# Kernel optimization log

Measured on AMD Instinct MI355X. Metric: run time of the kernel, lower is better.

The kernel has to match this reference:

```python
import jax, jax.numpy as jnp
import numpy as np

D_IN = 768      # encoder feature dim (hardcoded in GRUCell(768, d_model))
D_MODEL = 256   # hidden size
B, T = 64, 512


def _gru_cell(x, h, W_ih, W_hh, b_ih, b_hh):
    # PyTorch GRUCell math. W_ih: [in, 3H], W_hh: [H, 3H], biases [3H].
    gi = x @ W_ih + b_ih
    gh = h @ W_hh + b_hh
    i_r, i_z, i_n = jnp.split(gi, 3, axis=-1)
    h_r, h_z, h_n = jnp.split(gh, 3, axis=-1)
    r = jax.nn.sigmoid(i_r + h_r)
    z = jax.nn.sigmoid(i_z + h_z)
    n = jnp.tanh(i_n + r * h_n)
    return (1.0 - z) * n + z * h


def setup_inputs() -> dict:
    key = jax.random.key(0)
    ks = jax.random.split(key, 10)
    s_in = 1.0 / np.sqrt(D_MODEL)
    inp = {
        "encoder_outputs": jax.random.normal(ks[0], (B, T, D_IN), jnp.float32),
        "tau1": jnp.array([1.0], jnp.float32),
        "tau2": jnp.array([1.2], jnp.float32),
        "W_ih1": jax.random.normal(ks[1], (D_IN, 3 * D_MODEL), jnp.float32) * s_in,
        "W_hh1": jax.random.normal(ks[2], (D_MODEL, 3 * D_MODEL), jnp.float32) * s_in,
        "b_ih1": jax.random.normal(ks[3], (3 * D_MODEL,), jnp.float32) * s_in,
        "b_hh1": jax.random.normal(ks[4], (3 * D_MODEL,), jnp.float32) * s_in,
        "W_ih2": jax.random.normal(ks[5], (D_IN + D_MODEL, 3 * D_MODEL), jnp.float32) * s_in,
        "W_hh2": jax.random.normal(ks[6], (D_MODEL, 3 * D_MODEL), jnp.float32) * s_in,
        "b_ih2": jax.random.normal(ks[7], (3 * D_MODEL,), jnp.float32) * s_in,
        "b_hh2": jax.random.normal(ks[8], (3 * D_MODEL,), jnp.float32) * s_in,
    }
    return inp


def reference(encoder_outputs, tau1, tau2, W_ih1, W_hh1, b_ih1, b_hh1,
              W_ih2, W_hh2, b_ih2, b_hh2):
    bsz = encoder_outputs.shape[0]
    inv_t1 = 1.0 / tau1  # [1], broadcasts over [B, H]
    inv_t2 = 1.0 / tau2
    h0 = (jnp.zeros((bsz, D_MODEL), encoder_outputs.dtype),
          jnp.zeros((bsz, D_MODEL), encoder_outputs.dtype))

    xs = jnp.swapaxes(encoder_outputs, 0, 1)  # [T, B, D_IN]

    def step(carry, x_t):
        h1, h2 = carry
        h1_ = _gru_cell(x_t, h1, W_ih1, W_hh1, b_ih1, b_hh1)
        h1 = (1.0 - inv_t1) * h1 + inv_t1 * h1_
        x2 = jnp.concatenate([x_t, h1], axis=1)
        h2_ = _gru_cell(x2, h2, W_ih2, W_hh2, b_ih2, b_hh2)
        h2 = (1.0 - inv_t2) * h2 + inv_t2 * h2_
        return (h1, h2), (h1, h2)

    _, (o1, o2) = jax.lax.scan(step, h0, xs)  # each [T, B, H]
    out = jnp.concatenate([o1, o2], axis=2)   # [T, B, 2H]
    out = jnp.swapaxes(out, 0, 1)             # [B, T, 2H]
    # Note: F.dropout(p=0.5) in the original is stochastic; omitted here
    # (identity) so the reference is deterministic for kernel comparison.
    return out
```

## Files before the change

kernel.cpp:

```cpp
#include <hip/hip_runtime.h>

typedef _Float16 f16;
typedef _Float16 f16x2 __attribute__((ext_vector_type(2)));
typedef _Float16 f16x8 __attribute__((ext_vector_type(8)));
typedef float f32x4 __attribute__((ext_vector_type(4)));
typedef unsigned int u32;
typedef unsigned short u16;

#define B_SZ 64
#define T_SZ 512
#define DIN 768
#define H_SZ 256
#define TH 768
#define M_ROWS (B_SZ * T_SZ)

#define O_WT1 ((size_t)0)
#define O_WT2 (O_WT1 + (size_t)768 * 768 * 2)
#define O_H1 (O_WT2 + (size_t)768 * 1024 * 2)
#define O_G (O_H1 + (size_t)M_ROWS * H_SZ * 2)

__device__ __forceinline__ u32 pk2(float a, float b) {
  union { f16 h[2]; u32 u; } x;
  x.h[0] = (f16)a;
  x.h[1] = (f16)b;
  return x.u;
}

__device__ __forceinline__ float dot2f(u32 w, u32 h, float acc) {
#if __has_builtin(__builtin_amdgcn_fdot2)
  union { u32 u; f16x2 v; } a, b;
  a.u = w;
  b.u = h;
  return __builtin_amdgcn_fdot2(a.v, b.v, acc, false);
#else
  union { u32 u; f16 h[2]; } a, b;
  a.u = w;
  b.u = h;
  acc = fmaf((float)a.h[0], (float)b.h[0], acc);
  acc = fmaf((float)a.h[1], (float)b.h[1], acc);
  return acc;
#endif
}

__device__ __forceinline__ float sigmf_(float x) {
  return 1.0f / (1.0f + __expf(-x));
}
__device__ __forceinline__ float tanhf_(float x) {
  float e = __expf(-2.0f * fabsf(x));
  float r = (1.0f - e) / (1.0f + e);
  return copysignf(r, x);
}

__global__ __launch_bounds__(256) void k_transpose(const float* __restrict__ W,
                                                   f16* __restrict__ Wt, int K,
                                                   int N) {
  __shared__ f16 tile[32][33];
  int tx = threadIdx.x, ty = threadIdx.y;
  int n0 = blockIdx.x * 32, k0 = blockIdx.y * 32;
#pragma unroll
  for (int q = 0; q < 4; ++q) {
    int k = k0 + ty + q * 8;
    tile[ty + q * 8][tx] = (f16)W[(size_t)k * N + n0 + tx];
  }
  __syncthreads();
#pragma unroll
  for (int q = 0; q < 4; ++q) {
    int n = n0 + ty + q * 8;
    Wt[(size_t)n * K + k0 + tx] = tile[tx][ty + q * 8];
  }
}

#define LDK 40
__global__ __launch_bounds__(256, 2) void k_gemm(
    const float* __restrict__ A32, const f16* __restrict__ AH,
    const f16* __restrict__ Bt, const float* __restrict__ bias,
    f16* __restrict__ C, int K, int bstride) {
  __shared__ __align__(16) f16 Asm[128 * LDK];
  __shared__ __align__(16) f16 Bsm[128 * LDK];
  int tid = threadIdx.x;
  int lane = tid & 63, wave = tid >> 6;
  int wm = wave & 1, wn = wave >> 1;
  int fm = lane & 15, fk = (lane >> 4) * 8;
  int srow = tid >> 1, skp = (tid & 1) * 16;
  size_t r0 = (size_t)blockIdx.y * 128;
  int n0 = blockIdx.x * 128;
  f32x4 acc[4][4] = {};

  for (int k0 = 0; k0 < K; k0 += 32) {
    __syncthreads();
    if (k0 < DIN) {
      const float* src = A32 + (r0 + srow) * DIN + k0 + skp;
      float4 v0 = *(const float4*)(src);
      float4 v1 = *(const float4*)(src + 4);
      float4 v2 = *(const float4*)(src + 8);
      float4 v3 = *(const float4*)(src + 12);
      uint4 w0 = make_uint4(pk2(v0.x, v0.y), pk2(v0.z, v0.w), pk2(v1.x, v1.y),
                            pk2(v1.z, v1.w));
      uint4 w1 = make_uint4(pk2(v2.x, v2.y), pk2(v2.z, v2.w), pk2(v3.x, v3.y),
                            pk2(v3.z, v3.w));
      *(uint4*)&Asm[srow * LDK + skp] = w0;
      *(uint4*)&Asm[srow * LDK + skp + 8] = w1;
    } else {
      const uint4* src =
          (const uint4*)(AH + (r0 + srow) * H_SZ + (k0 - DIN) + skp);
      *(uint4*)&Asm[srow * LDK + skp] = src[0];
      *(uint4*)&Asm[srow * LDK + skp + 8] = src[1];
    }
    const uint4* bsrc =
        (const uint4*)(Bt + (size_t)(n0 + srow) * bstride + k0 + skp);
    *(uint4*)&Bsm[srow * LDK + skp] = bsrc[0];
    *(uint4*)&Bsm[srow * LDK + skp + 8] = bsrc[1];
    __syncthreads();

    f16x8 af[4], bf[4];
#pragma unroll
    for (int mt = 0; mt < 4; ++mt)
      af[mt] = *(const f16x8*)&Asm[(wm * 64 + mt * 16 + fm) * LDK + fk];
#pragma unroll
    for (int nt = 0; nt < 4; ++nt)
      bf[nt] = *(const f16x8*)&Bsm[(wn * 64 + nt * 16 + fm) * LDK + fk];
#pragma unroll
    for (int mt = 0; mt < 4; ++mt)
#pragma unroll
      for (int nt = 0; nt < 4; ++nt)
        acc[mt][nt] = __builtin_amdgcn_mfma_f32_16x16x32_f16(af[mt], bf[nt],
                                                             acc[mt][nt], 0, 0, 0);
  }

  int ccol = lane & 15, crb = (lane >> 4) * 4;
#pragma unroll
  for (int nt = 0; nt < 4; ++nt) {
    int col = n0 + wn * 64 + nt * 16 + ccol;
    float bv = bias[col];
#pragma unroll
    for (int mt = 0; mt < 4; ++mt) {
      size_t rb = r0 + wm * 64 + mt * 16 + crb;
#pragma unroll
      for (int rg = 0; rg < 4; ++rg)
        C[(rb + rg) * TH + col] = (f16)(acc[mt][nt][rg] + bv);
    }
  }
}

__global__ __launch_bounds__(512)
__attribute__((amdgpu_waves_per_eu(2, 2))) void k_rec(
    const f16* __restrict__ G, const float* __restrict__ Whh,
    const float* __restrict__ bhh, const float* __restrict__ tau,
    float* __restrict__ out, int out_off, f16* __restrict__ H1out) {
  __shared__ __align__(16) u16 s_h16[2][256];
  __shared__ float s_p0[256], s_p1[256], s_p2[256];

  const int tid = threadIdx.x;
  const int b = blockIdx.x;
  const int cg = tid & 255;
  const int kh = tid >> 8;

  uint4 w0[16], w1[16], w2[16];
  {
    const float* base = Whh + (size_t)(kh * 128) * TH + cg;
#pragma unroll
    for (int jj = 0; jj < 16; ++jj) {
      uint4 a, bq, c;
#pragma unroll
      for (int q = 0; q < 4; ++q) {
        const float* p = base + (size_t)(8 * jj + 2 * q) * TH;
        ((u32*)&a)[q] = pk2(p[0], p[TH]);
        ((u32*)&bq)[q] = pk2(p[256], p[TH + 256]);
        ((u32*)&c)[q] = pk2(p[512], p[TH + 512]);
      }
      w0[jj] = a;
      w1[jj] = bq;
      w2[jj] = c;
      if ((jj & 3) == 3) __builtin_amdgcn_sched_barrier(0);
    }
  }

  const float bb0 = bhh[cg], bb1 = bhh[cg + 256], bb2 = bhh[cg + 512];
  const float invt = 1.0f / tau[0];
  const float om = 1.0f - invt;

  if (tid < 256) s_h16[0][cg] = 0;

  const f16* gbase = G + (size_t)b * T_SZ * TH + cg;
  float* obase = out + (size_t)b * T_SZ * 512 + out_off + cg;
  f16* hbase = H1out ? H1out + (size_t)b * T_SZ * H_SZ + cg : (f16*)0;

  float hreg = 0.0f;
  f16 g0 = (f16)0.f, g1 = (f16)0.f, g2 = (f16)0.f;
  if (tid < 256) {
    g0 = gbase[0];
    g1 = gbase[256];
    g2 = gbase[512];
  }
  __syncthreads();

  for (int t = 0; t < T_SZ; ++t) {
    f16 n0 = (f16)0.f, n1 = (f16)0.f, n2 = (f16)0.f;
    {
      const int tn = (t + 1 < T_SZ) ? t + 1 : t;
      if (tid < 256) {
        const f16* gp = gbase + (size_t)tn * TH;
        n0 = gp[0];
        n1 = gp[256];
        n2 = gp[512];
      }
    }

    const uint4* hv4 = (const uint4*)(&s_h16[t & 1][0]) + kh * 16;
    float a0 = 0.f, a1 = 0.f, a2 = 0.f;
#pragma unroll
    for (int ii = 0; ii < 16; ++ii) {
      uint4 hv = hv4[ii];
      a0 = dot2f(w0[ii].x, hv.x, a0);
      a1 = dot2f(w1[ii].x, hv.x, a1);
      a2 = dot2f(w2[ii].x, hv.x, a2);
      a0 = dot2f(w0[ii].y, hv.y, a0);
      a1 = dot2f(w1[ii].y, hv.y, a1);
      a2 = dot2f(w2[ii].y, hv.y, a2);
      a0 = dot2f(w0[ii].z, hv.z, a0);
      a1 = dot2f(w1[ii].z, hv.z, a1);
      a2 = dot2f(w2[ii].z, hv.z, a2);
      a0 = dot2f(w0[ii].w, hv.w, a0);
      a1 = dot2f(w1[ii].w, hv.w, a1);
      a2 = dot2f(w2[ii].w, hv.w, a2);
    }

    if (kh) {
      s_p0[cg] = a0;
      s_p1[cg] = a1;
      s_p2[cg] = a2;
    }
    __syncthreads();

    if (tid < 256) {
      float ghr = a0 + s_p0[cg] + bb0;
      float ghz = a1 + s_p1[cg] + bb1;
      float ghn = a2 + s_p2[cg] + bb2;
      float r = sigmf_((float)g0 + ghr);
      float z = sigmf_((float)g1 + ghz);
      float n = tanhf_((float)g2 + r * ghn);
      float hc = (1.0f - z) * n + z * hreg;
      hreg = om * hreg + invt * hc;
      union { f16 h; u16 s; } hb;
      hb.h = (f16)hreg;
      s_h16[(t + 1) & 1][cg] = hb.s;
      obase[(size_t)t * 512] = hreg;
      if (hbase) hbase[(size_t)t * H_SZ] = (f16)hreg;
    }
    g0 = n0;
    g1 = n1;
    g2 = n2;
    __syncthreads();
  }
}

extern "C" void kernel_launch(void* const* d_in, const int* in_sizes, int n_in,
                              void* d_out, int out_size, void* d_ws,
                              size_t ws_size, hipStream_t stream) {
  const float* enc = (const float*)d_in[0];
  const float* tau1 = (const float*)d_in[1];
  const float* tau2 = (const float*)d_in[2];
  const float* Wih1 = (const float*)d_in[3];
  const float* Whh1 = (const float*)d_in[4];
  const float* bih1 = (const float*)d_in[5];
  const float* bhh1 = (const float*)d_in[6];
  const float* Wih2 = (const float*)d_in[7];
  const float* Whh2 = (const float*)d_in[8];
  const float* bih2 = (const float*)d_in[9];
  const float* bhh2 = (const float*)d_in[10];
  float* out = (float*)d_out;
  char* ws = (char*)d_ws;

  f16* Wt1 = (f16*)(ws + O_WT1);
  f16* Wt2 = (f16*)(ws + O_WT2);
  f16* H1 = (f16*)(ws + O_H1);
  f16* G = (f16*)(ws + O_G);

  k_transpose<<<dim3(24, 24), dim3(32, 8), 0, stream>>>(Wih1, Wt1, 768, 768);
  k_transpose<<<dim3(24, 32), dim3(32, 8), 0, stream>>>(Wih2, Wt2, 1024, 768);

  k_gemm<<<dim3(6, 256), 256, 0, stream>>>(enc, (const f16*)0, Wt1, bih1, G,
                                           768, 768);
  k_rec<<<64, 512, 0, stream>>>(G, Whh1, bhh1, tau1, out, 0, H1);

  k_gemm<<<dim3(6, 256), 256, 0, stream>>>(enc, H1, Wt2, bih2, G, 1024, 1024);
  k_rec<<<64, 512, 0, stream>>>(G, Whh2, bhh2, tau2, out, 256, (f16*)0);
}
```

Baseline: 1.680 ms.

## Split recurrent hidden-state reduction across four thread groups per block

The recurrent kernel now uses 1024 threads per block instead of 512. Each of four groups of 256 threads holds a quarter of W_hh in registers (96 u32 per thread instead of 192) and computes partial dot products over 64 hidden inputs, and the partial sums are reduced through shared memory. This halves the serial dot-product chain per timestep and the register pressure per thread. In exchange, each step adds more shared-memory traffic, a three-way reduction and a barrier across 16 waves instead of 8.

```diff
diff --git a/kernel.cpp b/kernel.cpp
--- a/kernel.cpp
+++ b/kernel.cpp
@@ -142,44 +142,37 @@
   }
 }
 
-__global__ __launch_bounds__(512)
-__attribute__((amdgpu_waves_per_eu(2, 2))) void k_rec(
+__global__ __launch_bounds__(1024)
+__attribute__((amdgpu_waves_per_eu(4, 4))) void k_rec(
     const f16* __restrict__ G, const float* __restrict__ Whh,
     const float* __restrict__ bhh, const float* __restrict__ tau,
     float* __restrict__ out, int out_off, f16* __restrict__ H1out) {
   __shared__ __align__(16) u16 s_h16[2][256];
-  __shared__ float s_p0[256], s_p1[256], s_p2[256];
+  __shared__ float s_p0[3][256], s_p1[3][256], s_p2[3][256];
 
   const int tid = threadIdx.x;
   const int b = blockIdx.x;
   const int cg = tid & 255;
-  const int kh = tid >> 8;
-
-  uint4 w0[16], w1[16], w2[16];
+  const int kq = tid >> 8;
+
+  if (tid < 256) s_h16[0][cg] = 0;
+
+  u32 w0[32], w1[32], w2[32];
   {
-    const float* base = Whh + (size_t)(kh * 128) * TH + cg;
-#pragma unroll
-    for (int jj = 0; jj < 16; ++jj) {
-      uint4 a, bq, c;
-#pragma unroll
-      for (int q = 0; q < 4; ++q) {
-        const float* p = base + (size_t)(8 * jj + 2 * q) * TH;
-        ((u32*)&a)[q] = pk2(p[0], p[TH]);
-        ((u32*)&bq)[q] = pk2(p[256], p[TH + 256]);
-        ((u32*)&c)[q] = pk2(p[512], p[TH + 512]);
-      }
-      w0[jj] = a;
-      w1[jj] = bq;
-      w2[jj] = c;
-      if ((jj & 3) == 3) __builtin_amdgcn_sched_barrier(0);
+    const float* base = Whh + (size_t)(kq * 64) * TH + cg;
+#pragma unroll
+    for (int j = 0; j < 32; ++j) {
+      const float* p = base + (size_t)(2 * j) * TH;
+      w0[j] = pk2(p[0], p[TH]);
+      w1[j] = pk2(p[256], p[TH + 256]);
+      w2[j] = pk2(p[512], p[TH + 512]);
+      if ((j & 7) == 7) __builtin_amdgcn_sched_barrier(0);
     }
   }
 
   const float bb0 = bhh[cg], bb1 = bhh[cg + 256], bb2 = bhh[cg + 512];
   const float invt = 1.0f / tau[0];
   const float om = 1.0f - invt;
-
-  if (tid < 256) s_h16[0][cg] = 0;
 
   const f16* gbase = G + (size_t)b * T_SZ * TH + cg;
   float* obase = out + (size_t)b * T_SZ * 512 + out_off + cg;
@@ -206,36 +199,36 @@
       }
     }
 
-    const uint4* hv4 = (const uint4*)(&s_h16[t & 1][0]) + kh * 16;
+    const uint4* hv4 = (const uint4*)(&s_h16[t & 1][0]) + kq * 8;
     float a0 = 0.f, a1 = 0.f, a2 = 0.f;
 #pragma unroll
-    for (int ii = 0; ii < 16; ++ii) {
+    for (int ii = 0; ii < 8; ++ii) {
       uint4 hv = hv4[ii];
-      a0 = dot2f(w0[ii].x, hv.x, a0);
-      a1 = dot2f(w1[ii].x, hv.x, a1);
-      a2 = dot2f(w2[ii].x, hv.x, a2);
-      a0 = dot2f(w0[ii].y, hv.y, a0);
-      a1 = dot2f(w1[ii].y, hv.y, a1);
-      a2 = dot2f(w2[ii].y, hv.y, a2);
-      a0 = dot2f(w0[ii].z, hv.z, a0);
-      a1 = dot2f(w1[ii].z, hv.z, a1);
-      a2 = dot2f(w2[ii].z, hv.z, a2);
-      a0 = dot2f(w0[ii].w, hv.w, a0);
-      a1 = dot2f(w1[ii].w, hv.w, a1);
-      a2 = dot2f(w2[ii].w, hv.w, a2);
-    }
-
-    if (kh) {
-      s_p0[cg] = a0;
-      s_p1[cg] = a1;
-      s_p2[cg] = a2;
+      a0 = dot2f(w0[4 * ii + 0], hv.x, a0);
+      a1 = dot2f(w1[4 * ii + 0], hv.x, a1);
+      a2 = dot2f(w2[4 * ii + 0], hv.x, a2);
+      a0 = dot2f(w0[4 * ii + 1], hv.y, a0);
+      a1 = dot2f(w1[4 * ii + 1], hv.y, a1);
+      a2 = dot2f(w2[4 * ii + 1], hv.y, a2);
+      a0 = dot2f(w0[4 * ii + 2], hv.z, a0);
+      a1 = dot2f(w1[4 * ii + 2], hv.z, a1);
+      a2 = dot2f(w2[4 * ii + 2], hv.z, a2);
+      a0 = dot2f(w0[4 * ii + 3], hv.w, a0);
+      a1 = dot2f(w1[4 * ii + 3], hv.w, a1);
+      a2 = dot2f(w2[4 * ii + 3], hv.w, a2);
+    }
+
+    if (kq) {
+      s_p0[kq - 1][cg] = a0;
+      s_p1[kq - 1][cg] = a1;
+      s_p2[kq - 1][cg] = a2;
     }
     __syncthreads();
 
     if (tid < 256) {
-      float ghr = a0 + s_p0[cg] + bb0;
-      float ghz = a1 + s_p1[cg] + bb1;
-      float ghn = a2 + s_p2[cg] + bb2;
+      float ghr = a0 + s_p0[0][cg] + s_p0[1][cg] + s_p0[2][cg] + bb0;
+      float ghz = a1 + s_p1[0][cg] + s_p1[1][cg] + s_p1[2][cg] + bb1;
+      float ghn = a2 + s_p2[0][cg] + s_p2[1][cg] + s_p2[2][cg] + bb2;
       float r = sigmf_((float)g0 + ghr);
       float z = sigmf_((float)g1 + ghz);
       float n = tanhf_((float)g2 + r * ghn);
@@ -281,8 +274,8 @@
 
   k_gemm<<<dim3(6, 256), 256, 0, stream>>>(enc, (const f16*)0, Wt1, bih1, G,
                                            768, 768);
-  k_rec<<<64, 512, 0, stream>>>(G, Whh1, bhh1, tau1, out, 0, H1);
+  k_rec<<<64, 1024, 0, stream>>>(G, Whh1, bhh1, tau1, out, 0, H1);
 
   k_gemm<<<dim3(6, 256), 256, 0, stream>>>(enc, H1, Wt2, bih2, G, 1024, 1024);
-  k_rec<<<64, 512, 0, stream>>>(G, Whh2, bhh2, tau2, out, 256, (f16*)0);
-}
+  k_rec<<<64, 1024, 0, stream>>>(G, Whh2, bhh2, tau2, out, 256, (f16*)0);
+}
```

Result: slower. 2.817 ms (+67.7%).
